# Optimization experiments

Hardware: AMD Instinct MI355X
Metric: run time of the kernel (lower is better)

## Reference

```python
import jax, jax.numpy as jnp
import numpy as np

B, T, C, HS = 8, 2048, 1024, 64

def setup_inputs() -> dict:
    key = jax.random.key(0)
    kx, kq, kk, kv = jax.random.split(key, 4)
    x = jax.random.normal(kx, (B, T, C), dtype=jnp.float32)
    # Linear(C, HS, bias=False) weights, stored as [C, HS] so projection is x @ W
    Wq = jax.random.normal(kq, (C, HS), dtype=jnp.float32) * (C ** -0.5)
    Wk = jax.random.normal(kk, (C, HS), dtype=jnp.float32) * (C ** -0.5)
    Wv = jax.random.normal(kv, (C, HS), dtype=jnp.float32) * (C ** -0.5)
    return {"x": x, "Wq": Wq, "Wk": Wk, "Wv": Wv}

def reference(x, Wq, Wk, Wv):
    Bq, Tq, Cq = x.shape
    q = x @ Wq  # [B,T,HS]
    k = x @ Wk
    v = x @ Wv
    # NOTE: original scales by C**-0.5 with C = embedding_dim (not head_size)
    att = jnp.einsum('bqd,bkd->bqk', q, k) * (Cq ** -0.5)  # [B,T,T]
    causal = jnp.tril(jnp.ones((Tq, Tq), dtype=bool))
    att = jnp.where(causal, att, -jnp.inf)
    att = jax.nn.softmax(att, axis=-1)
    # dropout p=0.0 -> identity
    y = jnp.einsum('bqk,bkd->bqd', att, v)  # [B,T,HS]
    return y
```

## Files before the change

kernel.cpp:

```cpp
#include <hip/hip_runtime.h>
#include <hip/hip_bf16.h>
#include <math.h>

#define B_   8
#define T_   2048
#define C_   1024
#define HS_  64
#define MTOT (B_*T_)

typedef __attribute__((ext_vector_type(8))) short bf16x8;
typedef __attribute__((ext_vector_type(4))) float f32x4;
typedef __attribute__((ext_vector_type(8))) unsigned short u16x8;

static __device__ __forceinline__ unsigned short f2bf(float f) {
    __hip_bfloat16 h = __float2bfloat16(f);
    return *reinterpret_cast<unsigned short*>(&h);
}

__global__ __launch_bounds__(256) void cast_w_kernel(
    const float* __restrict__ Wq, const float* __restrict__ Wk,
    const float* __restrict__ Wv, unsigned short* __restrict__ Wt)
{
    const int tid = threadIdx.x;
    const int col = tid & 63;
    const int kc  = tid >> 6;
    const int mat = blockIdx.y;
    const int k0  = (blockIdx.x * 4 + kc) * 8;
    const float* __restrict__ W = (mat == 0) ? Wq : (mat == 1) ? Wk : Wv;
    const float s = (mat == 0) ? 0.03125f : 1.0f;

    u16x8 o;
#pragma unroll
    for (int i = 0; i < 8; ++i)
        o[i] = f2bf(W[(size_t)(k0 + i) * HS_ + col] * s);
    *(u16x8*)&Wt[(size_t)(mat * 64 + col) * C_ + k0] = o;
}

__global__ __launch_bounds__(512) void proj_gemm(
    const float* __restrict__ x, const unsigned short* __restrict__ Wt,
    unsigned short* __restrict__ qbf, unsigned short* __restrict__ kbf,
    unsigned short* __restrict__ vtbf)
{
    __shared__ unsigned short Als[2][64][72];
    __shared__ unsigned short Bls[2][192][72];

    const int tid  = threadIdx.x;
    const int lane = tid & 63;
    const int wv   = tid >> 6;
    const int wr   = wv & 1;
    const int cg   = wv >> 1;
    const int g    = lane >> 4;
    const int n15  = lane & 15;
    const int g4   = g * 4;
    const int m0   = blockIdx.x * 64;

    const int srow = tid >> 3;
    const int seg  = (tid & 7) * 8;
    const float* __restrict__ xrow = &x[(size_t)(m0 + srow) * C_ + seg];
    const unsigned short* __restrict__ wrow = &Wt[(size_t)srow * C_ + seg];

    f32x4 acc[2][3];
#pragma unroll
    for (int i = 0; i < 2; ++i)
#pragma unroll
        for (int j = 0; j < 3; ++j) acc[i][j] = (f32x4){0.f, 0.f, 0.f, 0.f};

    float4 a0, a1;
    int4   b0, b1, b2;

#define PROJ_LOAD(KC)                                                   \
    do {                                                                \
        a0 = *(const float4*)&xrow[(KC) * 64 + 0];                      \
        a1 = *(const float4*)&xrow[(KC) * 64 + 4];                      \
        b0 = *(const int4*)&wrow[(KC) * 64];                            \
        b1 = *(const int4*)&wrow[(size_t)64  * C_ + (KC) * 64];        \
        b2 = *(const int4*)&wrow[(size_t)128 * C_ + (KC) * 64];        \
    } while (0)

#define PROJ_WRITE(BUF)                                                 \
    do {                                                                \
        u16x8 v0;                                                       \
        v0[0]=f2bf(a0.x); v0[1]=f2bf(a0.y); v0[2]=f2bf(a0.z); v0[3]=f2bf(a0.w); \
        v0[4]=f2bf(a1.x); v0[5]=f2bf(a1.y); v0[6]=f2bf(a1.z); v0[7]=f2bf(a1.w); \
        *(u16x8*)&Als[BUF][srow][seg]       = v0;                       \
        *(int4*)&Bls[BUF][srow][seg]        = b0;                       \
        *(int4*)&Bls[BUF][srow + 64][seg]   = b1;                       \
        *(int4*)&Bls[BUF][srow + 128][seg]  = b2;                       \
    } while (0)

    PROJ_LOAD(0);
    PROJ_WRITE(0);
    __syncthreads();

    for (int kc = 0; kc < C_ / 64; ++kc) {
        const int cur = kc & 1;
        const int kn  = (kc + 1 < C_ / 64) ? kc + 1 : kc;
        PROJ_LOAD(kn);

#pragma unroll
        for (int kk = 0; kk < 2; ++kk) {
            bf16x8 fa0 = *(const bf16x8*)&Als[cur][wr * 32 + n15][kk * 32 + g * 8];
            bf16x8 fa1 = *(const bf16x8*)&Als[cur][wr * 32 + 16 + n15][kk * 32 + g * 8];
            bf16x8 fb0 = *(const bf16x8*)&Bls[cur][cg * 48 + n15][kk * 32 + g * 8];
            bf16x8 fb1 = *(const bf16x8*)&Bls[cur][cg * 48 + 16 + n15][kk * 32 + g * 8];
            bf16x8 fb2 = *(const bf16x8*)&Bls[cur][cg * 48 + 32 + n15][kk * 32 + g * 8];
            acc[0][0] = __builtin_amdgcn_mfma_f32_16x16x32_bf16(fa0, fb0, acc[0][0], 0, 0, 0);
            acc[0][1] = __builtin_amdgcn_mfma_f32_16x16x32_bf16(fa0, fb1, acc[0][1], 0, 0, 0);
            acc[0][2] = __builtin_amdgcn_mfma_f32_16x16x32_bf16(fa0, fb2, acc[0][2], 0, 0, 0);
            acc[1][0] = __builtin_amdgcn_mfma_f32_16x16x32_bf16(fa1, fb0, acc[1][0], 0, 0, 0);
            acc[1][1] = __builtin_amdgcn_mfma_f32_16x16x32_bf16(fa1, fb1, acc[1][1], 0, 0, 0);
            acc[1][2] = __builtin_amdgcn_mfma_f32_16x16x32_bf16(fa1, fb2, acc[1][2], 0, 0, 0);
        }

        if (kc + 1 < C_ / 64) {
            __syncthreads();
            PROJ_WRITE(cur ^ 1);
            __syncthreads();
        }
    }
#undef PROJ_LOAD
#undef PROJ_WRITE

    __syncthreads();
    unsigned short* Cqk = &Als[0][0][0];
    unsigned short* Vtr = &Bls[0][0][0];

#pragma unroll
    for (int i = 0; i < 2; ++i)
#pragma unroll
        for (int j = 0; j < 3; ++j) {
            const int gcol = cg * 48 + j * 16 + n15;
            const int row0 = wr * 32 + i * 16 + g4;
            if (gcol < 128) {
#pragma unroll
                for (int r = 0; r < 4; ++r)
                    Cqk[(size_t)(row0 + r) * 136 + gcol] = f2bf(acc[i][j][r]);
            } else {
                ushort4 o;
                o.x = f2bf(acc[i][j][0]); o.y = f2bf(acc[i][j][1]);
                o.z = f2bf(acc[i][j][2]); o.w = f2bf(acc[i][j][3]);
                *(ushort4*)&Vtr[(size_t)(gcol - 128) * 72 + row0] = o;
            }
        }
    __syncthreads();

#pragma unroll
    for (int p = 0; p < 2; ++p) {
        const int flat = tid + p * 512;
        const int mat  = flat >> 9;
        const int r64  = (flat >> 3) & 63;
        const int sg   = (flat & 7) * 8;
        unsigned short* __restrict__ dst = mat ? kbf : qbf;
        *(int4*)&dst[(size_t)(m0 + r64) * HS_ + sg] =
            *(const int4*)&Cqk[(size_t)r64 * 136 + mat * 64 + sg];
    }
    {
        const int b  = m0 >> 11;
        const int t0 = m0 & 2047;
        const int hs = tid >> 3;
        *(int4*)&vtbf[((size_t)b * HS_ + hs) * T_ + t0 + seg] =
            *(const int4*)&Vtr[(size_t)hs * 72 + seg];
    }
}

__global__ __launch_bounds__(512) void attn_kernel(
    const unsigned short* __restrict__ qbf,
    const unsigned short* __restrict__ kbf,
    const unsigned short* __restrict__ vtbf,
    float* __restrict__ y)
{
    __shared__ unsigned short KVs[4][64][72];

    const int tid  = threadIdx.x;
    const int lane = tid & 63;
    const int wv   = tid >> 6;
    const int rg   = wv & 1;
    const int h    = (wv >> 1) & 1;
    const int tp   = wv >> 2;
    const int g    = lane >> 4;
    const int n15  = lane & 15;
    const int g4   = g * 4;
    const int b    = blockIdx.y;
    const size_t qkoff = (size_t)b * T_ * HS_;
    const size_t voff  = (size_t)b * HS_ * T_;

    const int sgrp = tid >> 8;
    const int st   = tid & 255;
    const int srow = st >> 3;
    const int soff = (st & 7) * 8;

    const unsigned short* __restrict__ kgb = &kbf[qkoff];
    const unsigned short* __restrict__ vgb = &vtbf[voff];

    for (int pass = 0; pass < 2; ++pass) {
        const int qbi  = pass ? (63 - (int)blockIdx.x) : (int)blockIdx.x;
        const int q0   = qbi * 32;
        const int qq0  = q0 + rg * 16;
        const int qrow = qq0 + n15;
        const int nkt  = (qbi >> 1) + 1;

        bf16x8 qf0 = *(const bf16x8*)&qbf[qkoff + (size_t)qrow * HS_ + g * 8];
        bf16x8 qf1 = *(const bf16x8*)&qbf[qkoff + (size_t)qrow * HS_ + g * 8 + 32];

        f32x4 o0 = {0.f,0.f,0.f,0.f}, o1 = o0, o2 = o0, o3 = o0;
        float mrow = -INFINITY, lrow = 0.f;

        int4 kr0, kr1, vr0, vr1;
        {
            int tix = (sgrp < nkt) ? sgrp : nkt - 1;
            kr0 = *(const int4*)&kgb[(size_t)(tix * 64 + srow) * HS_ + soff];
            kr1 = *(const int4*)&kgb[(size_t)(tix * 64 + srow + 32) * HS_ + soff];
            vr0 = *(const int4*)&vgb[(size_t)srow * T_ + tix * 64 + soff];
            vr1 = *(const int4*)&vgb[(size_t)(srow + 32) * T_ + tix * 64 + soff];
        }
        __syncthreads();
        *(int4*)&KVs[sgrp][srow][soff]          = kr0;
        *(int4*)&KVs[sgrp][srow + 32][soff]     = kr1;
        *(int4*)&KVs[2 + sgrp][srow][soff]      = vr0;
        *(int4*)&KVs[2 + sgrp][srow + 32][soff] = vr1;
        __syncthreads();

        const int J = (nkt + 1) >> 1;
        for (int j = 0; j < J; ++j) {
            const int kt = 2 * j + tp;
            {
                int tix = 2 * j + sgrp + 2;
                if (tix > nkt - 1) tix = nkt - 1;
                kr0 = *(const int4*)&kgb[(size_t)(tix * 64 + srow) * HS_ + soff];
                kr1 = *(const int4*)&kgb[(size_t)(tix * 64 + srow + 32) * HS_ + soff];
                vr0 = *(const int4*)&vgb[(size_t)srow * T_ + tix * 64 + soff];
                vr1 = *(const int4*)&vgb[(size_t)(srow + 32) * T_ + tix * 64 + soff];
            }

            if (kt < nkt) {
                const int k0  = kt * 64;
                const int ks0 = h * 32;
                f32x4 st0 = {0.f,0.f,0.f,0.f}, st1 = st0;
                {
                    bf16x8 ka;
                    ka  = *(const bf16x8*)&KVs[tp][ks0 + n15][g * 8];
                    st0 = __builtin_amdgcn_mfma_f32_16x16x32_bf16(ka, qf0, st0, 0, 0, 0);
                    ka  = *(const bf16x8*)&KVs[tp][ks0 + n15][g * 8 + 32];
                    st0 = __builtin_amdgcn_mfma_f32_16x16x32_bf16(ka, qf1, st0, 0, 0, 0);
                    ka  = *(const bf16x8*)&KVs[tp][ks0 + 16 + n15][g * 8];
                    st1 = __builtin_amdgcn_mfma_f32_16x16x32_bf16(ka, qf0, st1, 0, 0, 0);
                    ka  = *(const bf16x8*)&KVs[tp][ks0 + 16 + n15][g * 8 + 32];
                    st1 = __builtin_amdgcn_mfma_f32_16x16x32_bf16(ka, qf1, st1, 0, 0, 0);
                }

                const int kb = k0 + h * 32 + g4;
#pragma unroll
                for (int r = 0; r < 4; ++r) {
                    if (kb + r      > qrow) st0[r] = -INFINITY;
                    if (kb + 16 + r > qrow) st1[r] = -INFINITY;
                }

                float mloc = fmaxf(fmaxf(st0[0], st0[1]), fmaxf(st0[2], st0[3]));
                mloc = fmaxf(mloc, fmaxf(fmaxf(st1[0], st1[1]), fmaxf(st1[2], st1[3])));
                mloc = fmaxf(mloc, __shfl_xor(mloc, 16));
                mloc = fmaxf(mloc, __shfl_xor(mloc, 32));
                float mnew = fmaxf(mrow, mloc);
                float mb   = fmaxf(mnew, -1e30f);
                float corr = __expf(mrow - mb);
                float p[8];
                float psum = 0.f;
#pragma unroll
                for (int r = 0; r < 4; ++r) {
                    p[r]     = __expf(st0[r] - mb);
                    p[4 + r] = __expf(st1[r] - mb);
                    psum += p[r] + p[4 + r];
                }
                psum += __shfl_xor(psum, 16);
                psum += __shfl_xor(psum, 32);
                lrow = lrow * corr + psum;
                mrow = mnew;

#pragma unroll
                for (int r = 0; r < 4; ++r) {
                    float cr = __shfl(corr, g4 + r);
                    o0[r] *= cr; o1[r] *= cr; o2[r] *= cr; o3[r] *= cr;
                }

                bf16x8 pa;
#pragma unroll
                for (int r = 0; r < 4; ++r) {
                    pa[r]     = (short)f2bf(p[r]);
                    pa[4 + r] = (short)f2bf(p[4 + r]);
                }

                const int kvo = h * 32;
                {
                    ushort4 lo, hi; bf16x8 vb;
#define PV_STEP(NT, ONT)                                                        \
                    lo = *(const ushort4*)&KVs[2 + tp][(NT)*16 + n15][kvo + g4];\
                    hi = *(const ushort4*)&KVs[2 + tp][(NT)*16 + n15][kvo + 16 + g4];\
                    vb[0] = (short)lo.x; vb[1] = (short)lo.y;                   \
                    vb[2] = (short)lo.z; vb[3] = (short)lo.w;                   \
                    vb[4] = (short)hi.x; vb[5] = (short)hi.y;                   \
                    vb[6] = (short)hi.z; vb[7] = (short)hi.w;                   \
                    ONT = __builtin_amdgcn_mfma_f32_16x16x32_bf16(pa, vb, ONT, 0, 0, 0);
                    PV_STEP(0, o0)
                    PV_STEP(1, o1)
                    PV_STEP(2, o2)
                    PV_STEP(3, o3)
#undef PV_STEP
                }
            }

            if (j + 1 < J) {
                __syncthreads();
                *(int4*)&KVs[sgrp][srow][soff]          = kr0;
                *(int4*)&KVs[sgrp][srow + 32][soff]     = kr1;
                *(int4*)&KVs[2 + sgrp][srow][soff]      = vr0;
                *(int4*)&KVs[2 + sgrp][srow + 32][soff] = vr1;
                __syncthreads();
            }
        }

        __syncthreads();
        float* FS = (float*)&KVs[0][0][0];
        const int pid = (tp << 1) | h;
        if (pid != 0) {
            float* Ob = FS + (pid - 1) * 2176 + rg * 1088;
#pragma unroll
            for (int r = 0; r < 4; ++r) {
                Ob[(g4 + r) * 68 +  0 + n15] = o0[r];
                Ob[(g4 + r) * 68 + 16 + n15] = o1[r];
                Ob[(g4 + r) * 68 + 32 + n15] = o2[r];
                Ob[(g4 + r) * 68 + 48 + n15] = o3[r];
            }
            if (g == 0) {
                FS[6528 + (pid - 1) * 32 + rg * 16 + n15] = mrow;
                FS[6624 + (pid - 1) * 32 + rg * 16 + n15] = lrow;
            }
        }
        __syncthreads();
        if (pid == 0) {
            float m1 = FS[6528 +  0 + rg * 16 + n15];
            float m2 = FS[6528 + 32 + rg * 16 + n15];
            float m3 = FS[6528 + 64 + rg * 16 + n15];
            float l1 = FS[6624 +  0 + rg * 16 + n15];
            float l2 = FS[6624 + 32 + rg * 16 + n15];
            float l3 = FS[6624 + 64 + rg * 16 + n15];
            float mm = fmaxf(fmaxf(mrow, m1), fmaxf(m2, m3));
            float f0 = __expf(mrow - mm);
            float f1 = __expf(m1 - mm);
            float f2 = __expf(m2 - mm);
            float f3 = __expf(m3 - mm);
            float invl = 1.0f / (lrow * f0 + l1 * f1 + l2 * f2 + l3 * f3);
            const float* O1s = FS;
            const float* O2s = FS + 2176;
            const float* O3s = FS + 4352;
#pragma unroll
            for (int r = 0; r < 4; ++r) {
                float fr0 = __shfl(f0, g4 + r);
                float fr1 = __shfl(f1, g4 + r);
                float fr2 = __shfl(f2, g4 + r);
                float fr3 = __shfl(f3, g4 + r);
                float ir  = __shfl(invl, g4 + r);
                const int base = rg * 1088 + (g4 + r) * 68 + n15;
                float* yr = &y[((size_t)b * T_ + qq0 + g4 + r) * HS_];
                yr[ 0 + n15] = (o0[r] * fr0 + O1s[base]      * fr1 +
                                O2s[base]      * fr2 + O3s[base]      * fr3) * ir;
                yr[16 + n15] = (o1[r] * fr0 + O1s[base + 16] * fr1 +
                                O2s[base + 16] * fr2 + O3s[base + 16] * fr3) * ir;
                yr[32 + n15] = (o2[r] * fr0 + O1s[base + 32] * fr1 +
                                O2s[base + 32] * fr2 + O3s[base + 32] * fr3) * ir;
                yr[48 + n15] = (o3[r] * fr0 + O1s[base + 48] * fr1 +
                                O2s[base + 48] * fr2 + O3s[base + 48] * fr3) * ir;
            }
        }
    }
}

extern "C" void kernel_launch(void* const* d_in, const int* in_sizes, int n_in,
                              void* d_out, int out_size, void* d_ws, size_t ws_size,
                              hipStream_t stream)
{
    const float* x  = (const float*)d_in[0];
    const float* Wq = (const float*)d_in[1];
    const float* Wk = (const float*)d_in[2];
    const float* Wv = (const float*)d_in[3];

    unsigned short* qbf  = (unsigned short*)d_ws;
    unsigned short* kbf  = qbf + (size_t)MTOT * HS_;
    unsigned short* vtbf = kbf + (size_t)MTOT * HS_;
    unsigned short* Wt   = vtbf + (size_t)MTOT * HS_;

    cast_w_kernel<<<dim3(32, 3), 256, 0, stream>>>(Wq, Wk, Wv, Wt);
    proj_gemm<<<256, 512, 0, stream>>>(x, Wt, qbf, kbf, vtbf);
    attn_kernel<<<dim3(32, B_), 512, 0, stream>>>(qbf, kbf, vtbf, (float*)d_out);
}
```

Measured before the change: 50.10 us.

## Read K and V fragments directly from global memory, dropping LDS staging

Removes the shared-memory double-buffered staging of K/V tiles and the two block-wide barriers per tile step. Each wave now loads its MFMA operands for K and transposed V straight from global memory, relying on L1/L2 for the reuse between waves. Shared memory shrinks to the final cross-wave reduction buffer. This trades fewer barriers and LDS traffic for more redundant and less coalesced global loads: the V reads are 8-byte strided accesses, and there is no prefetch overlap.

```diff
diff --git a/kernel.cpp b/kernel.cpp
--- a/kernel.cpp
+++ b/kernel.cpp
@@ -169,7 +169,7 @@
     const unsigned short* __restrict__ vtbf,
     float* __restrict__ y)
 {
-    __shared__ unsigned short KVs[4][64][72];
+    __shared__ float FS[6720];
 
     const int tid  = threadIdx.x;
     const int lane = tid & 63;
@@ -184,11 +184,6 @@
     const size_t qkoff = (size_t)b * T_ * HS_;
     const size_t voff  = (size_t)b * HS_ * T_;
 
-    const int sgrp = tid >> 8;
-    const int st   = tid & 255;
-    const int srow = st >> 3;
-    const int soff = (st & 7) * 8;
-
     const unsigned short* __restrict__ kgb = &kbf[qkoff];
     const unsigned short* __restrict__ vgb = &vtbf[voff];
 
@@ -205,120 +200,83 @@
         f32x4 o0 = {0.f,0.f,0.f,0.f}, o1 = o0, o2 = o0, o3 = o0;
         float mrow = -INFINITY, lrow = 0.f;
 
-        int4 kr0, kr1, vr0, vr1;
-        {
-            int tix = (sgrp < nkt) ? sgrp : nkt - 1;
-            kr0 = *(const int4*)&kgb[(size_t)(tix * 64 + srow) * HS_ + soff];
-            kr1 = *(const int4*)&kgb[(size_t)(tix * 64 + srow + 32) * HS_ + soff];
-            vr0 = *(const int4*)&vgb[(size_t)srow * T_ + tix * 64 + soff];
-            vr1 = *(const int4*)&vgb[(size_t)(srow + 32) * T_ + tix * 64 + soff];
-        }
+        const int ks0 = h * 32;
+        for (int kt = tp; kt < nkt; kt += 2) {
+            const int k0   = kt * 64;
+            const int krow = k0 + ks0;
+
+            f32x4 st0 = {0.f,0.f,0.f,0.f}, st1 = st0;
+            {
+                bf16x8 ka0 = *(const bf16x8*)&kgb[(size_t)(krow + n15) * HS_ + g * 8];
+                bf16x8 ka1 = *(const bf16x8*)&kgb[(size_t)(krow + n15) * HS_ + g * 8 + 32];
+                bf16x8 ka2 = *(const bf16x8*)&kgb[(size_t)(krow + 16 + n15) * HS_ + g * 8];
+                bf16x8 ka3 = *(const bf16x8*)&kgb[(size_t)(krow + 16 + n15) * HS_ + g * 8 + 32];
+                st0 = __builtin_amdgcn_mfma_f32_16x16x32_bf16(ka0, qf0, st0, 0, 0, 0);
+                st0 = __builtin_amdgcn_mfma_f32_16x16x32_bf16(ka1, qf1, st0, 0, 0, 0);
+                st1 = __builtin_amdgcn_mfma_f32_16x16x32_bf16(ka2, qf0, st1, 0, 0, 0);
+                st1 = __builtin_amdgcn_mfma_f32_16x16x32_bf16(ka3, qf1, st1, 0, 0, 0);
+            }
+
+            const int kb = k0 + h * 32 + g4;
+#pragma unroll
+            for (int r = 0; r < 4; ++r) {
+                if (kb + r      > qrow) st0[r] = -INFINITY;
+                if (kb + 16 + r > qrow) st1[r] = -INFINITY;
+            }
+
+            float mloc = fmaxf(fmaxf(st0[0], st0[1]), fmaxf(st0[2], st0[3]));
+            mloc = fmaxf(mloc, fmaxf(fmaxf(st1[0], st1[1]), fmaxf(st1[2], st1[3])));
+            mloc = fmaxf(mloc, __shfl_xor(mloc, 16));
+            mloc = fmaxf(mloc, __shfl_xor(mloc, 32));
+            float mnew = fmaxf(mrow, mloc);
+            float mb   = fmaxf(mnew, -1e30f);
+            float corr = __expf(mrow - mb);
+            float p[8];
+            float psum = 0.f;
+#pragma unroll
+            for (int r = 0; r < 4; ++r) {
+                p[r]     = __expf(st0[r] - mb);
+                p[4 + r] = __expf(st1[r] - mb);
+                psum += p[r] + p[4 + r];
+            }
+            psum += __shfl_xor(psum, 16);
+            psum += __shfl_xor(psum, 32);
+            lrow = lrow * corr + psum;
+            mrow = mnew;
+
+#pragma unroll
+            for (int r = 0; r < 4; ++r) {
+                float cr = __shfl(corr, g4 + r);
+                o0[r] *= cr; o1[r] *= cr; o2[r] *= cr; o3[r] *= cr;
+            }
+
+            bf16x8 pa;
+#pragma unroll
+            for (int r = 0; r < 4; ++r) {
+                pa[r]     = (short)f2bf(p[r]);
+                pa[4 + r] = (short)f2bf(p[4 + r]);
+            }
+
+            const int kvo = k0 + h * 32;
+            {
+                ushort4 lo, hi; bf16x8 vb;
+#define PV_STEP(NT, ONT)                                                       \
+                lo = *(const ushort4*)&vgb[(size_t)((NT)*16 + n15) * T_ + kvo + g4];      \
+                hi = *(const ushort4*)&vgb[(size_t)((NT)*16 + n15) * T_ + kvo + 16 + g4]; \
+                vb[0] = (short)lo.x; vb[1] = (short)lo.y;                      \
+                vb[2] = (short)lo.z; vb[3] = (short)lo.w;                      \
+                vb[4] = (short)hi.x; vb[5] = (short)hi.y;                      \
+                vb[6] = (short)hi.z; vb[7] = (short)hi.w;                      \
+                ONT = __builtin_amdgcn_mfma_f32_16x16x32_bf16(pa, vb, ONT, 0, 0, 0);
+                PV_STEP(0, o0)
+                PV_STEP(1, o1)
+                PV_STEP(2, o2)
+                PV_STEP(3, o3)
+#undef PV_STEP
+            }
+        }
+
         __syncthreads();
-        *(int4*)&KVs[sgrp][srow][soff]          = kr0;
-        *(int4*)&KVs[sgrp][srow + 32][soff]     = kr1;
-        *(int4*)&KVs[2 + sgrp][srow][soff]      = vr0;
-        *(int4*)&KVs[2 + sgrp][srow + 32][soff] = vr1;
-        __syncthreads();
-
-        const int J = (nkt + 1) >> 1;
-        for (int j = 0; j < J; ++j) {
-            const int kt = 2 * j + tp;
-            {
-                int tix = 2 * j + sgrp + 2;
-                if (tix > nkt - 1) tix = nkt - 1;
-                kr0 = *(const int4*)&kgb[(size_t)(tix * 64 + srow) * HS_ + soff];
-                kr1 = *(const int4*)&kgb[(size_t)(tix * 64 + srow + 32) * HS_ + soff];
-                vr0 = *(const int4*)&vgb[(size_t)srow * T_ + tix * 64 + soff];
-                vr1 = *(const int4*)&vgb[(size_t)(srow + 32) * T_ + tix * 64 + soff];
-            }
-
-            if (kt < nkt) {
-                const int k0  = kt * 64;
-                const int ks0 = h * 32;
-                f32x4 st0 = {0.f,0.f,0.f,0.f}, st1 = st0;
-                {
-                    bf16x8 ka;
-                    ka  = *(const bf16x8*)&KVs[tp][ks0 + n15][g * 8];
-                    st0 = __builtin_amdgcn_mfma_f32_16x16x32_bf16(ka, qf0, st0, 0, 0, 0);
-                    ka  = *(const bf16x8*)&KVs[tp][ks0 + n15][g * 8 + 32];
-                    st0 = __builtin_amdgcn_mfma_f32_16x16x32_bf16(ka, qf1, st0, 0, 0, 0);
-                    ka  = *(const bf16x8*)&KVs[tp][ks0 + 16 + n15][g * 8];
-                    st1 = __builtin_amdgcn_mfma_f32_16x16x32_bf16(ka, qf0, st1, 0, 0, 0);
-                    ka  = *(const bf16x8*)&KVs[tp][ks0 + 16 + n15][g * 8 + 32];
-                    st1 = __builtin_amdgcn_mfma_f32_16x16x32_bf16(ka, qf1, st1, 0, 0, 0);
-                }
-
-                const int kb = k0 + h * 32 + g4;
-#pragma unroll
-                for (int r = 0; r < 4; ++r) {
-                    if (kb + r      > qrow) st0[r] = -INFINITY;
-                    if (kb + 16 + r > qrow) st1[r] = -INFINITY;
-                }
-
-                float mloc = fmaxf(fmaxf(st0[0], st0[1]), fmaxf(st0[2], st0[3]));
-                mloc = fmaxf(mloc, fmaxf(fmaxf(st1[0], st1[1]), fmaxf(st1[2], st1[3])));
-                mloc = fmaxf(mloc, __shfl_xor(mloc, 16));
-                mloc = fmaxf(mloc, __shfl_xor(mloc, 32));
-                float mnew = fmaxf(mrow, mloc);
-                float mb   = fmaxf(mnew, -1e30f);
-                float corr = __expf(mrow - mb);
-                float p[8];
-                float psum = 0.f;
-#pragma unroll
-                for (int r = 0; r < 4; ++r) {
-                    p[r]     = __expf(st0[r] - mb);
-                    p[4 + r] = __expf(st1[r] - mb);
-                    psum += p[r] + p[4 + r];
-                }
-                psum += __shfl_xor(psum, 16);
-                psum += __shfl_xor(psum, 32);
-                lrow = lrow * corr + psum;
-                mrow = mnew;
-
-#pragma unroll
-                for (int r = 0; r < 4; ++r) {
-                    float cr = __shfl(corr, g4 + r);
-                    o0[r] *= cr; o1[r] *= cr; o2[r] *= cr; o3[r] *= cr;
-                }
-
-                bf16x8 pa;
-#pragma unroll
-                for (int r = 0; r < 4; ++r) {
-                    pa[r]     = (short)f2bf(p[r]);
-                    pa[4 + r] = (short)f2bf(p[4 + r]);
-                }
-
-                const int kvo = h * 32;
-                {
-                    ushort4 lo, hi; bf16x8 vb;
-#define PV_STEP(NT, ONT)                                                        \
-                    lo = *(const ushort4*)&KVs[2 + tp][(NT)*16 + n15][kvo + g4];\
-                    hi = *(const ushort4*)&KVs[2 + tp][(NT)*16 + n15][kvo + 16 + g4];\
-                    vb[0] = (short)lo.x; vb[1] = (short)lo.y;                   \
-                    vb[2] = (short)lo.z; vb[3] = (short)lo.w;                   \
-                    vb[4] = (short)hi.x; vb[5] = (short)hi.y;                   \
-                    vb[6] = (short)hi.z; vb[7] = (short)hi.w;                   \
-                    ONT = __builtin_amdgcn_mfma_f32_16x16x32_bf16(pa, vb, ONT, 0, 0, 0);
-                    PV_STEP(0, o0)
-                    PV_STEP(1, o1)
-                    PV_STEP(2, o2)
-                    PV_STEP(3, o3)
-#undef PV_STEP
-                }
-            }
-
-            if (j + 1 < J) {
-                __syncthreads();
-                *(int4*)&KVs[sgrp][srow][soff]          = kr0;
-                *(int4*)&KVs[sgrp][srow + 32][soff]     = kr1;
-                *(int4*)&KVs[2 + sgrp][srow][soff]      = vr0;
-                *(int4*)&KVs[2 + sgrp][srow + 32][soff] = vr1;
-                __syncthreads();
-            }
-        }
-
-        __syncthreads();
-        float* FS = (float*)&KVs[0][0][0];
         const int pid = (tp << 1) | h;
         if (pid != 0) {
             float* Ob = FS + (pid - 1) * 2176 + rg * 1088;
```

Measured after the change: 74.81 us. 49.3% more time.
